# Optimization experiments

Hardware: AMD Instinct MI355X
Metric: run time of the kernel (lower is better)

Reference implementation:

```python
import jax, jax.numpy as jnp
import numpy as np

D, H, E, K, DF = 1024, 16, 8, 2, 4096
HD = D // H


def setup_inputs() -> dict:
    key = jax.random.key(0)
    ks = jax.random.split(key, 16)
    s = 0.02
    return {
        "x": jax.random.normal(ks[0], (8, 1024, D), jnp.float32),
        "ln1_g": jnp.ones((D,), jnp.float32),
        "ln1_b": jnp.zeros((D,), jnp.float32),
        "Wqkv": jax.random.normal(ks[1], (D, 3 * D), jnp.float32) * s,
        "bqkv": jnp.zeros((3 * D,), jnp.float32),
        "Wo": jax.random.normal(ks[2], (D, D), jnp.float32) * s,
        "bo": jnp.zeros((D,), jnp.float32),
        "ln2_g": jnp.ones((D,), jnp.float32),
        "ln2_b": jnp.zeros((D,), jnp.float32),
        "Wr": jax.random.normal(ks[3], (D, E), jnp.float32) * s,
        "W1": jax.random.normal(ks[4], (E, D, DF), jnp.float32) * s,
        "b1": jnp.zeros((E, DF), jnp.float32),
        "W2": jax.random.normal(ks[5], (E, DF, D), jnp.float32) * s,
        "b2": jnp.zeros((E, D), jnp.float32),
    }


def _ln(x, g, b, eps=1e-5):
    mu = jnp.mean(x, axis=-1, keepdims=True)
    var = jnp.var(x, axis=-1, keepdims=True)
    return (x - mu) * jax.lax.rsqrt(var + eps) * g + b


def reference(x, ln1_g, ln1_b, Wqkv, bqkv, Wo, bo, ln2_g, ln2_b, Wr, W1, b1, W2, b2):
    B, S, _ = x.shape
    # ---- pre-norm multi-head attention ----
    n1 = _ln(x, ln1_g, ln1_b)
    qkv = n1 @ Wqkv + bqkv  # [B,S,3D]
    q, k, v = jnp.split(qkv, 3, axis=-1)
    q = q.reshape(B, S, H, HD).transpose(0, 2, 1, 3)
    k = k.reshape(B, S, H, HD).transpose(0, 2, 1, 3)
    v = v.reshape(B, S, H, HD).transpose(0, 2, 1, 3)
    scores = jnp.einsum("bhqd,bhkd->bhqk", q, k) / np.sqrt(HD).astype(np.float32)
    attn = jax.nn.softmax(scores, axis=-1)
    ao = jnp.einsum("bhqk,bhkd->bhqd", attn, v)
    ao = ao.transpose(0, 2, 1, 3).reshape(B, S, D) @ Wo + bo
    x = x + ao  # residual (dropout=0)

    # ---- pre-norm MoE FFN ----
    n2 = _ln(x, ln2_g, ln2_b).reshape(B * S, D)  # [T,D]
    logits = n2 @ Wr  # [T,E]
    probs = jax.nn.softmax(logits, axis=-1)
    topv, topi = jax.lax.top_k(probs, K)  # [T,K]
    topv = topv / jnp.sum(topv, axis=-1, keepdims=True)
    onehot = jax.nn.one_hot(topi, E, dtype=probs.dtype)  # [T,K,E]
    gates = jnp.einsum("tke,tk->te", onehot, topv)  # dense sparse gates [T,E]

    # dense dispatch: each expert's FFN weighted by its gate (zero for unrouted)
    moe = jnp.zeros_like(n2)
    for e in range(E):
        h = jax.nn.gelu(n2 @ W1[e] + b1[e])
        moe = moe + gates[:, e:e + 1] * (h @ W2[e] + b2[e])
    x = x + moe.reshape(B, S, D)

    # load-balancing aux loss: E * sum(frac_routed_e * mean_prob_e)
    frac = jnp.mean(jnp.sum(onehot, axis=1), axis=0) / K  # [E]
    aux = E * jnp.sum(frac * jnp.mean(probs, axis=0))
    return x, aux
```

## Files before the change

kernel.cpp:

```cpp
#include <hip/hip_runtime.h>
#include <cstdint>
#include <cstddef>

using u16 = unsigned short;
using u32 = unsigned int;
typedef __attribute__((ext_vector_type(8))) short bf16x8;
typedef __attribute__((ext_vector_type(4))) float f32x4;

#define T_TOK 8192
#define SEQ   1024
#define NHEAD 16

__device__ __forceinline__ u16 f2b(float f) {
  u32 u = __float_as_uint(f);
  u32 r = (u + 0x7FFFu + ((u >> 16) & 1u)) >> 16;
  return (u16)r;
}
__device__ __forceinline__ float b2f(u16 u) {
  return __uint_as_float(((u32)u) << 16);
}
__device__ __forceinline__ u32 pk_bf16(float a, float b) {
  u32 r;
  asm("v_cvt_pk_bf16_f32 %0, %1, %2" : "=v"(r) : "v"(a), "v"(b));
  return r;
}

__global__ __launch_bounds__(256)
void k_cast_transpose(const float* __restrict__ in, u16* __restrict__ out, int R, int C) {
  __shared__ float tile[32][33];
  int bc = blockIdx.x * 32, br = blockIdx.y * 32;
  size_t bofs = (size_t)blockIdx.z * R * C;
  in += bofs; out += bofs;
  int tx = threadIdx.x, ty = threadIdx.y;
  for (int i = 0; i < 32; i += 8)
    tile[ty + i][tx] = in[(size_t)(br + ty + i) * C + bc + tx];
  __syncthreads();
  for (int i = 0; i < 32; i += 8)
    out[(size_t)(bc + ty + i) * R + br + tx] = f2b(tile[tx][ty + i]);
}

__global__ __launch_bounds__(256)
void k_ln(const float* __restrict__ x, const float* __restrict__ g, const float* __restrict__ b,
          u16* __restrict__ out) {
  int row = blockIdx.x, t = threadIdx.x;
  float4 v = ((const float4*)(x + (size_t)row * 1024))[t];
  float s  = v.x + v.y + v.z + v.w;
  float ss = v.x * v.x + v.y * v.y + v.z * v.z + v.w * v.w;
  for (int d = 1; d < 64; d <<= 1) { s += __shfl_xor(s, d); ss += __shfl_xor(ss, d); }
  __shared__ float sm[8];
  int w = t >> 6, lane = t & 63;
  if (lane == 0) { sm[w] = s; sm[4 + w] = ss; }
  __syncthreads();
  s = sm[0] + sm[1] + sm[2] + sm[3];
  ss = sm[4] + sm[5] + sm[6] + sm[7];
  float mu = s * (1.f / 1024.f);
  float var = ss * (1.f / 1024.f) - mu * mu;
  float inv = rsqrtf(var + 1e-5f);
  float4 gv = ((const float4*)g)[t];
  float4 bv = ((const float4*)b)[t];
  u32 lo = pk_bf16((v.x - mu) * inv * gv.x + bv.x, (v.y - mu) * inv * gv.y + bv.y);
  u32 hi = pk_bf16((v.z - mu) * inv * gv.z + bv.z, (v.w - mu) * inv * gv.w + bv.w);
  u32* dst = (u32*)(out + (size_t)row * 1024 + t * 4);
  dst[0] = lo; dst[1] = hi;
}

template<int MODE, bool EXPERT, bool GATHER>
__global__ __launch_bounds__(256)
void k_gemm(const u16* __restrict__ A, const u16* __restrict__ BT,
            const float* __restrict__ bias, const float* __restrict__ res,
            void* __restrict__ Cout, int M, int N, int Kd, int ldA,
            const int* __restrict__ off, const int* __restrict__ rows) {
  int nx = gridDim.x, ny = gridDim.y;
  int rid = blockIdx.x + nx * (blockIdx.y + ny * blockIdx.z);
  int z, bx, by;
  if (EXPERT) {
    z = rid & 7;
    int inner = rid >> 3;
    by = inner % ny;
    bx = inner / ny;
  } else {
    z = 0;
    int xcd = rid & 7;
    int inner = rid >> 3;
    bx = inner % nx;
    by = (inner / nx) * 8 + xcd;
  }
  int m_base = 0, M_local = M;
  if (EXPERT) { m_base = off[z]; M_local = off[z + 1] - m_base; }
  if (by * 128 >= M_local) return;
  if (EXPERT) { BT += (size_t)z * N * Kd; bias += (size_t)z * N; }

  __shared__ alignas(1024) u16 As[2][4096];
  __shared__ alignas(1024) u16 Bs[2][4096];

  int t = threadIdx.x;
  int lane = t & 63, w = t >> 6;
  int wm = w >> 1, wn = w & 1;
  int lr = lane & 15;
  int slot = lane >> 4;
  int sx = (slot ^ ((lr >> 1) & 3)) << 3;

  int ssrc = (lane & 3) ^ ((lane >> 3) & 3);
  const u16* aG[2]; const u16* bG[2];
  u16* aL[2]; u16* bL[2];
#pragma unroll
  for (int c = 0; c < 2; c++) {
    int chunk = 2 * w + c;
    int rl = chunk * 16 + (lane >> 2);
    int mr = by * 128 + rl;
    int mc = mr < M_local - 1 ? mr : M_local - 1;
    size_t arow = GATHER ? (size_t)rows[m_base + mc] : (size_t)(m_base + mc);
    aG[c] = A + arow * (size_t)ldA + ssrc * 8;
    bG[c] = BT + (size_t)(bx * 128 + rl) * Kd + ssrc * 8;
    aL[c] = &As[0][chunk * 512];
    bL[c] = &Bs[0][chunk * 512];
  }

  auto stage = [&](int k0, int buf) {
#pragma unroll
    for (int c = 0; c < 2; c++) {
      __builtin_amdgcn_global_load_lds(
          (const __attribute__((address_space(1))) void*)(aG[c] + k0),
          (__attribute__((address_space(3))) void*)(aL[c] + buf * 4096), 16, 0, 0);
      __builtin_amdgcn_global_load_lds(
          (const __attribute__((address_space(1))) void*)(bG[c] + k0),
          (__attribute__((address_space(3))) void*)(bL[c] + buf * 4096), 16, 0, 0);
    }
  };

  f32x4 acc[4][4] = {};

  stage(0, 0);
  __syncthreads();
  int cur = 0;
  for (int k0 = 0; k0 < Kd; k0 += 32) {
    if (k0 + 32 < Kd) stage(k0 + 32, cur ^ 1);
    bf16x8 af[4], bfr[4];
#pragma unroll
    for (int m = 0; m < 4; m++)
      af[m] = *(const bf16x8*)&As[cur][(wm * 64 + m * 16 + lr) * 32 + sx];
#pragma unroll
    for (int n = 0; n < 4; n++)
      bfr[n] = *(const bf16x8*)&Bs[cur][(wn * 64 + n * 16 + lr) * 32 + sx];
#pragma unroll
    for (int m = 0; m < 4; m++)
#pragma unroll
      for (int n = 0; n < 4; n++)
        acc[m][n] = __builtin_amdgcn_mfma_f32_16x16x32_bf16(af[m], bfr[n], acc[m][n], 0, 0, 0);
    __syncthreads();
    cur ^= 1;
  }

  int cr = (lane >> 4) * 4, cc = lane & 15;
#pragma unroll
  for (int m = 0; m < 4; m++) {
    int rl = by * 128 + wm * 64 + m * 16 + cr;
#pragma unroll
    for (int n = 0; n < 4; n++) {
      int col = bx * 128 + wn * 64 + n * 16 + cc;
      float bia = bias[col];
      float v0 = acc[m][n][0] + bia, v1 = acc[m][n][1] + bia;
      float v2 = acc[m][n][2] + bia, v3 = acc[m][n][3] + bia;
      if (MODE == 2) {
        const float cc2 = -2.3025850929940457f;
        float u0 = v0 + 0.044715f * v0 * v0 * v0;
        float u1 = v1 + 0.044715f * v1 * v1 * v1;
        float u2 = v2 + 0.044715f * v2 * v2 * v2;
        float u3 = v3 + 0.044715f * v3 * v3 * v3;
        v0 = v0 / (1.f + exp2f(cc2 * u0));
        v1 = v1 / (1.f + exp2f(cc2 * u1));
        v2 = v2 / (1.f + exp2f(cc2 * u2));
        v3 = v3 / (1.f + exp2f(cc2 * u3));
      }
      if (MODE == 0 || MODE == 2) {
        u32 p01 = pk_bf16(v0, v1), p23 = pk_bf16(v2, v3);
        u16* cp = (u16*)Cout;
        if (rl + 0 < M_local) cp[(size_t)(m_base + rl + 0) * N + col] = (u16)p01;
        if (rl + 1 < M_local) cp[(size_t)(m_base + rl + 1) * N + col] = (u16)(p01 >> 16);
        if (rl + 2 < M_local) cp[(size_t)(m_base + rl + 2) * N + col] = (u16)p23;
        if (rl + 3 < M_local) cp[(size_t)(m_base + rl + 3) * N + col] = (u16)(p23 >> 16);
      } else {
        float* cp = (float*)Cout;
        float vv[4] = {v0, v1, v2, v3};
#pragma unroll
        for (int r = 0; r < 4; r++) {
          int rr = rl + r;
          if (rr >= M_local) continue;
          size_t row = (size_t)(m_base + rr);
          if (MODE == 1) cp[row * N + col] = vv[r] + res[row * N + col];
          else           cp[row * N + col] = vv[r];
        }
      }
    }
  }
}

__global__ __launch_bounds__(256)
void k_attn(const u16* __restrict__ qkv, u16* __restrict__ ao) {
  __shared__ u16 Kt[64][72];
  __shared__ u16 Vt[64][72];
  __shared__ u16 Pl[4][16][72];

  int bh = blockIdx.y;
  int b = bh >> 4, h = bh & 15;
  int q0 = blockIdx.x * 64;
  int t = threadIdx.x, lane = t & 63, w = t >> 6;
  int lr = lane & 15, lk = (lane >> 4) * 8;

  int tq = b * SEQ + q0 + w * 16 + lr;
  const u16* qrow = qkv + (size_t)tq * 3072 + h * 64;
  bf16x8 qf[2];
#pragma unroll
  for (int kk = 0; kk < 2; kk++) {
    bf16x8 raw = *(const bf16x8*)(qrow + kk * 32 + lk);
#pragma unroll
    for (int j = 0; j < 8; j++) raw[j] = (short)f2b(b2f((u16)raw[j]) * 0.125f);
    qf[kk] = raw;
  }

  float m[4], l[4];
  f32x4 o[4];
#pragma unroll
  for (int r = 0; r < 4; r++) { m[r] = -1e30f; l[r] = 0.f; }
#pragma unroll
  for (int c = 0; c < 4; c++) o[c] = (f32x4){0.f, 0.f, 0.f, 0.f};

  int key_r = t >> 2;
  int key_c = (t & 3) * 16;

  for (int kv0 = 0; kv0 < SEQ; kv0 += 64) {
    int tk = b * SEQ + kv0 + key_r;
    const u16* krow = qkv + (size_t)tk * 3072 + 1024 + h * 64 + key_c;
    const u16* vrow = qkv + (size_t)tk * 3072 + 2048 + h * 64 + key_c;
    int4 ka = *(const int4*)krow;
    int4 kb = *(const int4*)(krow + 8);
    int4 vv4[2];
    vv4[0] = *(const int4*)vrow;
    vv4[1] = *(const int4*)(vrow + 8);
    const u16* vv = (const u16*)vv4;
    __syncthreads();
    *(int4*)&Kt[key_r][key_c] = ka;
    *(int4*)&Kt[key_r][key_c + 8] = kb;
#pragma unroll
    for (int j = 0; j < 16; j++) Vt[key_c + j][key_r] = vv[j];
    __syncthreads();

    f32x4 s[4];
#pragma unroll
    for (int n = 0; n < 4; n++) {
      s[n] = (f32x4){0.f, 0.f, 0.f, 0.f};
#pragma unroll
      for (int kk = 0; kk < 2; kk++) {
        bf16x8 kf = *(const bf16x8*)&Kt[n * 16 + lr][kk * 32 + lk];
        s[n] = __builtin_amdgcn_mfma_f32_16x16x32_bf16(qf[kk], kf, s[n], 0, 0, 0);
      }
    }
    float alpha[4], rsum[4];
#pragma unroll
    for (int r = 0; r < 4; r++) {
      float mx = fmaxf(fmaxf(s[0][r], s[1][r]), fmaxf(s[2][r], s[3][r]));
#pragma unroll
      for (int d = 1; d < 16; d <<= 1) mx = fmaxf(mx, __shfl_xor(mx, d));
      float mn = fmaxf(m[r], mx);
      alpha[r] = expf(m[r] - mn);
      m[r] = mn;
      rsum[r] = 0.f;
    }
#pragma unroll
    for (int n = 0; n < 4; n++)
#pragma unroll
      for (int r = 0; r < 4; r++) {
        float p = expf(s[n][r] - m[r]);
        rsum[r] += p;
        Pl[w][(lane >> 4) * 4 + r][n * 16 + lr] = f2b(p);
      }
#pragma unroll
    for (int r = 0; r < 4; r++) {
      float rs = rsum[r];
#pragma unroll
      for (int d = 1; d < 16; d <<= 1) rs += __shfl_xor(rs, d);
      l[r] = l[r] * alpha[r] + rs;
#pragma unroll
      for (int c = 0; c < 4; c++) o[c][r] *= alpha[r];
    }
    bf16x8 pa[2];
#pragma unroll
    for (int kk = 0; kk < 2; kk++) pa[kk] = *(const bf16x8*)&Pl[w][lr][kk * 32 + lk];
#pragma unroll
    for (int c = 0; c < 4; c++)
#pragma unroll
      for (int kk = 0; kk < 2; kk++) {
        bf16x8 vf = *(const bf16x8*)&Vt[c * 16 + lr][kk * 32 + lk];
        o[c] = __builtin_amdgcn_mfma_f32_16x16x32_bf16(pa[kk], vf, o[c], 0, 0, 0);
      }
  }

  int cr = (lane >> 4) * 4, cc = lane & 15;
#pragma unroll
  for (int r = 0; r < 4; r++) {
    float invl = 1.f / l[r];
    int trow = b * SEQ + q0 + w * 16 + cr + r;
#pragma unroll
    for (int c = 0; c < 4; c++)
      ao[(size_t)trow * 1024 + h * 64 + c * 16 + cc] = f2b(o[c][r] * invl);
  }
}

__global__ __launch_bounds__(256)
void k_router(const float* __restrict__ x1, const float* __restrict__ g, const float* __restrict__ b,
              const float* __restrict__ Wr, int* __restrict__ topi, float* __restrict__ topv,
              int* __restrict__ cnt_part, float* __restrict__ sp_part) {
  __shared__ int lcnt[8];
  __shared__ float lsp[8];
  int t = threadIdx.x, w = t >> 6, lane = t & 63;
  if (t < 8) { lcnt[t] = 0; lsp[t] = 0.f; }
  __syncthreads();

  float gv[16], bv[16];
#pragma unroll
  for (int i = 0; i < 4; i++) {
    float4 g4 = ((const float4*)g)[lane * 4 + i];
    float4 b4 = ((const float4*)b)[lane * 4 + i];
    gv[i * 4 + 0] = g4.x; gv[i * 4 + 1] = g4.y; gv[i * 4 + 2] = g4.z; gv[i * 4 + 3] = g4.w;
    bv[i * 4 + 0] = b4.x; bv[i * 4 + 1] = b4.y; bv[i * 4 + 2] = b4.z; bv[i * 4 + 3] = b4.w;
  }
  float wr[16][8];
#pragma unroll
  for (int j = 0; j < 16; j++) {
    float4 w0 = ((const float4*)Wr)[(lane * 16 + j) * 2];
    float4 w1 = ((const float4*)Wr)[(lane * 16 + j) * 2 + 1];
    wr[j][0] = w0.x; wr[j][1] = w0.y; wr[j][2] = w0.z; wr[j][3] = w0.w;
    wr[j][4] = w1.x; wr[j][5] = w1.y; wr[j][6] = w1.z; wr[j][7] = w1.w;
  }

  for (int i = 0; i < 8; i++) {
    int row = blockIdx.x * 32 + w * 8 + i;
    const float4* xr = (const float4*)(x1 + (size_t)row * 1024);
    float xv[16];
    float s = 0.f, ss = 0.f;
#pragma unroll
    for (int q = 0; q < 4; q++) {
      float4 v = xr[lane * 4 + q];
      xv[q * 4 + 0] = v.x; xv[q * 4 + 1] = v.y; xv[q * 4 + 2] = v.z; xv[q * 4 + 3] = v.w;
      s += v.x + v.y + v.z + v.w;
      ss += v.x * v.x + v.y * v.y + v.z * v.z + v.w * v.w;
    }
#pragma unroll
    for (int d = 1; d < 64; d <<= 1) { s += __shfl_xor(s, d); ss += __shfl_xor(ss, d); }
    float mu = s * (1.f / 1024.f);
    float var = ss * (1.f / 1024.f) - mu * mu;
    float inv = rsqrtf(var + 1e-5f);
    float p[8] = {};
#pragma unroll
    for (int j = 0; j < 16; j++) {
      float n = (xv[j] - mu) * inv * gv[j] + bv[j];
#pragma unroll
      for (int e = 0; e < 8; e++) p[e] += n * wr[j][e];
    }
#pragma unroll
    for (int e = 0; e < 8; e++)
#pragma unroll
      for (int d = 1; d < 64; d <<= 1) p[e] += __shfl_xor(p[e], d);
    if (lane == 0) {
      float mx = p[0];
#pragma unroll
      for (int e = 1; e < 8; e++) mx = fmaxf(mx, p[e]);
      float ex[8], sum = 0.f;
#pragma unroll
      for (int e = 0; e < 8; e++) { ex[e] = expf(p[e] - mx); sum += ex[e]; }
      float pr[8];
#pragma unroll
      for (int e = 0; e < 8; e++) pr[e] = ex[e] / sum;
      int i0 = 0; float b0 = pr[0];
      for (int e = 1; e < 8; e++) if (pr[e] > b0) { b0 = pr[e]; i0 = e; }
      int i1 = -1; float b1 = -1.f;
      for (int e = 0; e < 8; e++) if (e != i0 && pr[e] > b1) { b1 = pr[e]; i1 = e; }
      float inv2 = 1.f / (b0 + b1);
      topi[row * 2] = i0; topi[row * 2 + 1] = i1;
      topv[row * 2] = b0 * inv2; topv[row * 2 + 1] = b1 * inv2;
      atomicAdd(&lcnt[i0], 1); atomicAdd(&lcnt[i1], 1);
#pragma unroll
      for (int e = 0; e < 8; e++) atomicAdd(&lsp[e], pr[e]);
    }
  }
  __syncthreads();
  if (t < 8) {
    cnt_part[blockIdx.x * 8 + t] = lcnt[t];
    sp_part[blockIdx.x * 8 + t] = lsp[t];
  }
}

__global__ void k_scan_aux(const int* __restrict__ cnt_part, const float* __restrict__ sp_part,
                           int* __restrict__ off, int* __restrict__ cursor, float* __restrict__ aux_out) {
  __shared__ int csum[8];
  __shared__ float ssum[8];
  int t = threadIdx.x;
  int e = t & 7, ch = t >> 3;
  int c = 0; float s = 0.f;
  for (int i = ch * 32; i < ch * 32 + 32; i++) { c += cnt_part[i * 8 + e]; s += sp_part[i * 8 + e]; }
#pragma unroll
  for (int d = 8; d < 64; d <<= 1) { c += __shfl_xor(c, d); s += __shfl_xor(s, d); }
  if (t < 8) { csum[t] = c; ssum[t] = s; }
  __syncthreads();
  if (t == 0) {
    int o = 0;
    for (int q = 0; q < 8; q++) { off[q] = o; cursor[q] = o; o += csum[q]; }
    off[8] = o;
    float aux = 0.f;
    for (int q = 0; q < 8; q++)
      aux += ((float)csum[q] / (float)(T_TOK * 2)) * (ssum[q] / (float)T_TOK);
    aux_out[0] = 8.f * aux;
  }
}

__global__ __launch_bounds__(256)
void k_scatter(const int* __restrict__ topi, int* __restrict__ cursor,
               int* __restrict__ rows, int* __restrict__ slot_of) {
  __shared__ int hist[8];
  __shared__ int base[8];
  int t = threadIdx.x;
  if (t < 8) hist[t] = 0;
  __syncthreads();
  int tok = blockIdx.x * 256 + t;
  int e0 = topi[tok * 2], e1 = topi[tok * 2 + 1];
  int r0 = atomicAdd(&hist[e0], 1);
  int r1 = atomicAdd(&hist[e1], 1);
  __syncthreads();
  if (t < 8) base[t] = atomicAdd(&cursor[t], hist[t]);
  __syncthreads();
  int p0 = base[e0] + r0, p1 = base[e1] + r1;
  rows[p0] = tok; rows[p1] = tok;
  slot_of[tok * 2] = p0; slot_of[tok * 2 + 1] = p1;
}

__global__ __launch_bounds__(256)
void k_combine(const float* __restrict__ x1, const float* __restrict__ out2,
               const int* __restrict__ slot_of, const float* __restrict__ topv,
               float* __restrict__ out) {
  int row = blockIdx.x, t = threadIdx.x;
  int s0 = slot_of[row * 2], s1 = slot_of[row * 2 + 1];
  float w0 = topv[row * 2], w1 = topv[row * 2 + 1];
  float4 a  = ((const float4*)(x1 + (size_t)row * 1024))[t];
  float4 e0 = ((const float4*)(out2 + (size_t)s0 * 1024))[t];
  float4 e1 = ((const float4*)(out2 + (size_t)s1 * 1024))[t];
  float4 r;
  r.x = a.x + w0 * e0.x + w1 * e1.x;
  r.y = a.y + w0 * e0.y + w1 * e1.y;
  r.z = a.z + w0 * e0.z + w1 * e1.z;
  r.w = a.w + w0 * e0.w + w1 * e1.w;
  ((float4*)(out + (size_t)row * 1024))[t] = r;
}

extern "C" void kernel_launch(void* const* d_in, const int* in_sizes, int n_in,
                              void* d_out, int out_size, void* d_ws, size_t ws_size,
                              hipStream_t stream) {
  const float* x    = (const float*)d_in[0];
  const float* ln1g = (const float*)d_in[1];
  const float* ln1b = (const float*)d_in[2];
  const float* Wqkv = (const float*)d_in[3];
  const float* bqkv = (const float*)d_in[4];
  const float* Wo   = (const float*)d_in[5];
  const float* bo   = (const float*)d_in[6];
  const float* ln2g = (const float*)d_in[7];
  const float* ln2b = (const float*)d_in[8];
  const float* Wr   = (const float*)d_in[9];
  const float* W1   = (const float*)d_in[10];
  const float* b1   = (const float*)d_in[11];
  const float* W2   = (const float*)d_in[12];
  const float* b2   = (const float*)d_in[13];
  float* out = (float*)d_out;

  char* wp = (char*)d_ws;
  auto alloc = [&](size_t bytes) -> void* {
    void* p = (void*)wp;
    wp += (bytes + 255) & ~(size_t)255;
    return p;
  };
  u16*   WqkvT = (u16*)alloc((size_t)3072 * 1024 * 2);
  u16*   WoT   = (u16*)alloc((size_t)1024 * 1024 * 2);
  u16*   W1T   = (u16*)alloc((size_t)8 * 4096 * 1024 * 2);
  u16*   W2T   = (u16*)alloc((size_t)8 * 1024 * 4096 * 2);
  u16*   n1    = (u16*)alloc((size_t)8192 * 1024 * 2);
  u16*   qkv   = (u16*)alloc((size_t)8192 * 3072 * 2);
  u16*   aob   = (u16*)alloc((size_t)8192 * 1024 * 2);
  float* x1    = (float*)alloc((size_t)8192 * 1024 * 4);
  u16*   n2b   = (u16*)alloc((size_t)8192 * 1024 * 2);
  u16*   hbuf  = (u16*)alloc((size_t)16384 * 4096 * 2);
  float* out2  = (float*)alloc((size_t)16384 * 1024 * 4);
  int*   topi  = (int*)alloc((size_t)8192 * 2 * 4);
  float* topv  = (float*)alloc((size_t)8192 * 2 * 4);
  int*   rowsl = (int*)alloc((size_t)16384 * 4);
  int*   slot  = (int*)alloc((size_t)16384 * 4);
  int*   cntp  = (int*)alloc((size_t)256 * 8 * 4);
  float* spp   = (float*)alloc((size_t)256 * 8 * 4);
  int*   offs  = (int*)alloc(256);
  int*   curs  = (int*)alloc(256);

  k_cast_transpose<<<dim3(96, 32, 1), dim3(32, 8), 0, stream>>>(Wqkv, WqkvT, 1024, 3072);
  k_cast_transpose<<<dim3(32, 32, 1), dim3(32, 8), 0, stream>>>(Wo, WoT, 1024, 1024);
  k_cast_transpose<<<dim3(128, 32, 8), dim3(32, 8), 0, stream>>>(W1, W1T, 1024, 4096);
  k_cast_transpose<<<dim3(32, 128, 8), dim3(32, 8), 0, stream>>>(W2, W2T, 4096, 1024);

  k_ln<<<8192, 256, 0, stream>>>(x, ln1g, ln1b, n1);
  k_gemm<0, false, false><<<dim3(24, 64, 1), 256, 0, stream>>>(
      n1, WqkvT, bqkv, nullptr, qkv, 8192, 3072, 1024, 1024, nullptr, nullptr);
  k_attn<<<dim3(16, 128), 256, 0, stream>>>(qkv, aob);
  k_gemm<1, false, false><<<dim3(8, 64, 1), 256, 0, stream>>>(
      aob, WoT, bo, x, x1, 8192, 1024, 1024, 1024, nullptr, nullptr);

  k_ln<<<8192, 256, 0, stream>>>(x1, ln2g, ln2b, n2b);
  k_router<<<256, 256, 0, stream>>>(x1, ln2g, ln2b, Wr, topi, topv, cntp, spp);
  k_scan_aux<<<1, 64, 0, stream>>>(cntp, spp, offs, curs, out + 8388608);
  k_scatter<<<32, 256, 0, stream>>>(topi, curs, rowsl, slot);

  k_gemm<2, true, true><<<dim3(32, 64, 8), 256, 0, stream>>>(
      n2b, W1T, b1, nullptr, hbuf, 0, 4096, 1024, 1024, offs, rowsl);
  k_gemm<3, true, false><<<dim3(8, 64, 8), 256, 0, stream>>>(
      hbuf, W2T, b2, nullptr, out2, 0, 1024, 4096, 4096, offs, nullptr);
  k_combine<<<8192, 256, 0, stream>>>(x1, out2, slot, topv, out);
}
```

Before: 905.5 us.

## Fuse LN2 into router and make expert GEMMs loop over row tiles

The second LayerNorm is folded into the router kernel, which now writes the normalized bf16 activations while computing routing logits, removing a separate pass over x1. The GEMM kernel gains an outer loop over M-tiles with a grid stride, so the expert GEMMs launch a quarter as many row blocks and each block walks several row tiles. This cuts the many early-exit blocks for lightly loaded experts, at the cost of less parallelism and load imbalance when one expert gets many tokens.

```diff
diff --git a/kernel.cpp b/kernel.cpp
--- a/kernel.cpp
+++ b/kernel.cpp
@@ -72,22 +72,23 @@
             const int* __restrict__ off, const int* __restrict__ rows) {
   int nx = gridDim.x, ny = gridDim.y;
   int rid = blockIdx.x + nx * (blockIdx.y + ny * blockIdx.z);
-  int z, bx, by;
+  int z, bx, by0, bystep;
   if (EXPERT) {
     z = rid & 7;
     int inner = rid >> 3;
-    by = inner % ny;
+    by0 = inner % ny;
     bx = inner / ny;
+    bystep = ny;
   } else {
     z = 0;
     int xcd = rid & 7;
     int inner = rid >> 3;
     bx = inner % nx;
-    by = (inner / nx) * 8 + xcd;
+    by0 = (inner / nx) * 8 + xcd;
+    bystep = 1 << 20;
   }
   int m_base = 0, M_local = M;
   if (EXPERT) { m_base = off[z]; M_local = off[z + 1] - m_base; }
-  if (by * 128 >= M_local) return;
   if (EXPERT) { BT += (size_t)z * N * Kd; bias += (size_t)z * N; }
 
   __shared__ alignas(1024) u16 As[2][4096];
@@ -101,94 +102,100 @@
   int sx = (slot ^ ((lr >> 1) & 3)) << 3;
 
   int ssrc = (lane & 3) ^ ((lane >> 3) & 3);
-  const u16* aG[2]; const u16* bG[2];
-  u16* aL[2]; u16* bL[2];
+  const u16* bG[2];
+  int rlc[2], cofs[2];
 #pragma unroll
   for (int c = 0; c < 2; c++) {
     int chunk = 2 * w + c;
-    int rl = chunk * 16 + (lane >> 2);
-    int mr = by * 128 + rl;
-    int mc = mr < M_local - 1 ? mr : M_local - 1;
-    size_t arow = GATHER ? (size_t)rows[m_base + mc] : (size_t)(m_base + mc);
-    aG[c] = A + arow * (size_t)ldA + ssrc * 8;
-    bG[c] = BT + (size_t)(bx * 128 + rl) * Kd + ssrc * 8;
-    aL[c] = &As[0][chunk * 512];
-    bL[c] = &Bs[0][chunk * 512];
-  }
-
-  auto stage = [&](int k0, int buf) {
+    rlc[c] = chunk * 16 + (lane >> 2);
+    bG[c] = BT + (size_t)(bx * 128 + rlc[c]) * Kd + ssrc * 8;
+    cofs[c] = chunk * 512;
+  }
+
+  for (int by = by0; by * 128 < M_local; by += bystep) {
+    const u16* aG[2];
 #pragma unroll
     for (int c = 0; c < 2; c++) {
-      __builtin_amdgcn_global_load_lds(
-          (const __attribute__((address_space(1))) void*)(aG[c] + k0),
-          (__attribute__((address_space(3))) void*)(aL[c] + buf * 4096), 16, 0, 0);
-      __builtin_amdgcn_global_load_lds(
-          (const __attribute__((address_space(1))) void*)(bG[c] + k0),
-          (__attribute__((address_space(3))) void*)(bL[c] + buf * 4096), 16, 0, 0);
-    }
-  };
-
-  f32x4 acc[4][4] = {};
-
-  stage(0, 0);
-  __syncthreads();
-  int cur = 0;
-  for (int k0 = 0; k0 < Kd; k0 += 32) {
-    if (k0 + 32 < Kd) stage(k0 + 32, cur ^ 1);
-    bf16x8 af[4], bfr[4];
-#pragma unroll
-    for (int m = 0; m < 4; m++)
-      af[m] = *(const bf16x8*)&As[cur][(wm * 64 + m * 16 + lr) * 32 + sx];
-#pragma unroll
-    for (int n = 0; n < 4; n++)
-      bfr[n] = *(const bf16x8*)&Bs[cur][(wn * 64 + n * 16 + lr) * 32 + sx];
-#pragma unroll
-    for (int m = 0; m < 4; m++)
+      int mr = by * 128 + rlc[c];
+      int mc = mr < M_local - 1 ? mr : M_local - 1;
+      size_t arow = GATHER ? (size_t)rows[m_base + mc] : (size_t)(m_base + mc);
+      aG[c] = A + arow * (size_t)ldA + ssrc * 8;
+    }
+
+    auto stage = [&](int k0, int buf) {
+#pragma unroll
+      for (int c = 0; c < 2; c++) {
+        __builtin_amdgcn_global_load_lds(
+            (const __attribute__((address_space(1))) void*)(aG[c] + k0),
+            (__attribute__((address_space(3))) void*)(&As[buf][cofs[c]]), 16, 0, 0);
+        __builtin_amdgcn_global_load_lds(
+            (const __attribute__((address_space(1))) void*)(bG[c] + k0),
+            (__attribute__((address_space(3))) void*)(&Bs[buf][cofs[c]]), 16, 0, 0);
+      }
+    };
+
+    f32x4 acc[4][4] = {};
+
+    stage(0, 0);
+    __syncthreads();
+    int cur = 0;
+    for (int k0 = 0; k0 < Kd; k0 += 32) {
+      if (k0 + 32 < Kd) stage(k0 + 32, cur ^ 1);
+      bf16x8 af[4], bfr[4];
+#pragma unroll
+      for (int m = 0; m < 4; m++)
+        af[m] = *(const bf16x8*)&As[cur][(wm * 64 + m * 16 + lr) * 32 + sx];
 #pragma unroll
       for (int n = 0; n < 4; n++)
-        acc[m][n] = __builtin_amdgcn_mfma_f32_16x16x32_bf16(af[m], bfr[n], acc[m][n], 0, 0, 0);
-    __syncthreads();
-    cur ^= 1;
-  }
-
-  int cr = (lane >> 4) * 4, cc = lane & 15;
-#pragma unroll
-  for (int m = 0; m < 4; m++) {
-    int rl = by * 128 + wm * 64 + m * 16 + cr;
-#pragma unroll
-    for (int n = 0; n < 4; n++) {
-      int col = bx * 128 + wn * 64 + n * 16 + cc;
-      float bia = bias[col];
-      float v0 = acc[m][n][0] + bia, v1 = acc[m][n][1] + bia;
-      float v2 = acc[m][n][2] + bia, v3 = acc[m][n][3] + bia;
-      if (MODE == 2) {
-        const float cc2 = -2.3025850929940457f;
-        float u0 = v0 + 0.044715f * v0 * v0 * v0;
-        float u1 = v1 + 0.044715f * v1 * v1 * v1;
-        float u2 = v2 + 0.044715f * v2 * v2 * v2;
-        float u3 = v3 + 0.044715f * v3 * v3 * v3;
-        v0 = v0 / (1.f + exp2f(cc2 * u0));
-        v1 = v1 / (1.f + exp2f(cc2 * u1));
-        v2 = v2 / (1.f + exp2f(cc2 * u2));
-        v3 = v3 / (1.f + exp2f(cc2 * u3));
-      }
-      if (MODE == 0 || MODE == 2) {
-        u32 p01 = pk_bf16(v0, v1), p23 = pk_bf16(v2, v3);
-        u16* cp = (u16*)Cout;
-        if (rl + 0 < M_local) cp[(size_t)(m_base + rl + 0) * N + col] = (u16)p01;
-        if (rl + 1 < M_local) cp[(size_t)(m_base + rl + 1) * N + col] = (u16)(p01 >> 16);
-        if (rl + 2 < M_local) cp[(size_t)(m_base + rl + 2) * N + col] = (u16)p23;
-        if (rl + 3 < M_local) cp[(size_t)(m_base + rl + 3) * N + col] = (u16)(p23 >> 16);
-      } else {
-        float* cp = (float*)Cout;
-        float vv[4] = {v0, v1, v2, v3};
-#pragma unroll
-        for (int r = 0; r < 4; r++) {
-          int rr = rl + r;
-          if (rr >= M_local) continue;
-          size_t row = (size_t)(m_base + rr);
-          if (MODE == 1) cp[row * N + col] = vv[r] + res[row * N + col];
-          else           cp[row * N + col] = vv[r];
+        bfr[n] = *(const bf16x8*)&Bs[cur][(wn * 64 + n * 16 + lr) * 32 + sx];
+#pragma unroll
+      for (int m = 0; m < 4; m++)
+#pragma unroll
+        for (int n = 0; n < 4; n++)
+          acc[m][n] = __builtin_amdgcn_mfma_f32_16x16x32_bf16(af[m], bfr[n], acc[m][n], 0, 0, 0);
+      __syncthreads();
+      cur ^= 1;
+    }
+
+    int cr = (lane >> 4) * 4, cc = lane & 15;
+#pragma unroll
+    for (int m = 0; m < 4; m++) {
+      int rl = by * 128 + wm * 64 + m * 16 + cr;
+#pragma unroll
+      for (int n = 0; n < 4; n++) {
+        int col = bx * 128 + wn * 64 + n * 16 + cc;
+        float bia = bias[col];
+        float v0 = acc[m][n][0] + bia, v1 = acc[m][n][1] + bia;
+        float v2 = acc[m][n][2] + bia, v3 = acc[m][n][3] + bia;
+        if (MODE == 2) {
+          const float cc2 = -2.3025850929940457f;
+          float u0 = v0 + 0.044715f * v0 * v0 * v0;
+          float u1 = v1 + 0.044715f * v1 * v1 * v1;
+          float u2 = v2 + 0.044715f * v2 * v2 * v2;
+          float u3 = v3 + 0.044715f * v3 * v3 * v3;
+          v0 = v0 / (1.f + exp2f(cc2 * u0));
+          v1 = v1 / (1.f + exp2f(cc2 * u1));
+          v2 = v2 / (1.f + exp2f(cc2 * u2));
+          v3 = v3 / (1.f + exp2f(cc2 * u3));
+        }
+        if (MODE == 0 || MODE == 2) {
+          u32 p01 = pk_bf16(v0, v1), p23 = pk_bf16(v2, v3);
+          u16* cp = (u16*)Cout;
+          if (rl + 0 < M_local) cp[(size_t)(m_base + rl + 0) * N + col] = (u16)p01;
+          if (rl + 1 < M_local) cp[(size_t)(m_base + rl + 1) * N + col] = (u16)(p01 >> 16);
+          if (rl + 2 < M_local) cp[(size_t)(m_base + rl + 2) * N + col] = (u16)p23;
+          if (rl + 3 < M_local) cp[(size_t)(m_base + rl + 3) * N + col] = (u16)(p23 >> 16);
+        } else {
+          float* cp = (float*)Cout;
+          float vv[4] = {v0, v1, v2, v3};
+#pragma unroll
+          for (int r = 0; r < 4; r++) {
+            int rr = rl + r;
+            if (rr >= M_local) continue;
+            size_t row = (size_t)(m_base + rr);
+            if (MODE == 1) cp[row * N + col] = vv[r] + res[row * N + col];
+            else           cp[row * N + col] = vv[r];
+          }
         }
       }
     }
@@ -308,7 +315,8 @@
 
 __global__ __launch_bounds__(256)
 void k_router(const float* __restrict__ x1, const float* __restrict__ g, const float* __restrict__ b,
-              const float* __restrict__ Wr, int* __restrict__ topi, float* __restrict__ topv,
+              const float* __restrict__ Wr, u16* __restrict__ n2b,
+              int* __restrict__ topi, float* __restrict__ topv,
               int* __restrict__ cnt_part, float* __restrict__ sp_part) {
   __shared__ int lcnt[8];
   __shared__ float lsp[8];
@@ -354,8 +362,17 @@
 #pragma unroll
     for (int j = 0; j < 16; j++) {
       float n = (xv[j] - mu) * inv * gv[j] + bv[j];
+      xv[j] = n;
 #pragma unroll
       for (int e = 0; e < 8; e++) p[e] += n * wr[j][e];
+    }
+    {
+      u32 pk[8];
+#pragma unroll
+      for (int jj = 0; jj < 8; jj++) pk[jj] = pk_bf16(xv[2 * jj], xv[2 * jj + 1]);
+      uint4* dst = (uint4*)(n2b + (size_t)row * 1024 + lane * 16);
+      dst[0] = make_uint4(pk[0], pk[1], pk[2], pk[3]);
+      dst[1] = make_uint4(pk[4], pk[5], pk[6], pk[7]);
     }
 #pragma unroll
     for (int e = 0; e < 8; e++)
@@ -508,14 +525,13 @@
   k_gemm<1, false, false><<<dim3(8, 64, 1), 256, 0, stream>>>(
       aob, WoT, bo, x, x1, 8192, 1024, 1024, 1024, nullptr, nullptr);
 
-  k_ln<<<8192, 256, 0, stream>>>(x1, ln2g, ln2b, n2b);
-  k_router<<<256, 256, 0, stream>>>(x1, ln2g, ln2b, Wr, topi, topv, cntp, spp);
+  k_router<<<256, 256, 0, stream>>>(x1, ln2g, ln2b, Wr, n2b, topi, topv, cntp, spp);
   k_scan_aux<<<1, 64, 0, stream>>>(cntp, spp, offs, curs, out + 8388608);
   k_scatter<<<32, 256, 0, stream>>>(topi, curs, rowsl, slot);
 
-  k_gemm<2, true, true><<<dim3(32, 64, 8), 256, 0, stream>>>(
+  k_gemm<2, true, true><<<dim3(32, 16, 8), 256, 0, stream>>>(
       n2b, W1T, b1, nullptr, hbuf, 0, 4096, 1024, 1024, offs, rowsl);
-  k_gemm<3, true, false><<<dim3(8, 64, 8), 256, 0, stream>>>(
+  k_gemm<3, true, false><<<dim3(8, 16, 8), 256, 0, stream>>>(
       hbuf, W2T, b2, nullptr, out2, 0, 1024, 4096, 4096, offs, nullptr);
   k_combine<<<8192, 256, 0, stream>>>(x1, out2, slot, topv, out);
 }
```

New measurement: 1.042 ms. +15.1%, slower.

## Fuse LN2 bf16 output into router and store expert outputs as bf16

Applied to the files above, without the earlier changes.

The router kernel now writes the normalized bf16 activations itself, so the separate second layernorm launch and its extra read of x1 go away. The second expert GEMM switches to epilogue mode 0 and writes bf16 instead of fp32, halving the out2 buffer. The combine kernel reads the bf16 expert outputs and widens them. This cuts memory traffic in exchange for lower precision in the expert outputs, and mode 0 may add a bias differently than mode 3 did.

```diff
diff --git a/kernel.cpp b/kernel.cpp
--- a/kernel.cpp
+++ b/kernel.cpp
@@ -308,7 +308,8 @@
 
 __global__ __launch_bounds__(256)
 void k_router(const float* __restrict__ x1, const float* __restrict__ g, const float* __restrict__ b,
-              const float* __restrict__ Wr, int* __restrict__ topi, float* __restrict__ topv,
+              const float* __restrict__ Wr, u16* __restrict__ n2b,
+              int* __restrict__ topi, float* __restrict__ topv,
               int* __restrict__ cnt_part, float* __restrict__ sp_part) {
   __shared__ int lcnt[8];
   __shared__ float lsp[8];
@@ -354,8 +355,17 @@
 #pragma unroll
     for (int j = 0; j < 16; j++) {
       float n = (xv[j] - mu) * inv * gv[j] + bv[j];
+      xv[j] = n;
 #pragma unroll
       for (int e = 0; e < 8; e++) p[e] += n * wr[j][e];
+    }
+    {
+      u32 pk[8];
+#pragma unroll
+      for (int jj = 0; jj < 8; jj++) pk[jj] = pk_bf16(xv[2 * jj], xv[2 * jj + 1]);
+      uint4* dst = (uint4*)(n2b + (size_t)row * 1024 + lane * 16);
+      dst[0] = make_uint4(pk[0], pk[1], pk[2], pk[3]);
+      dst[1] = make_uint4(pk[4], pk[5], pk[6], pk[7]);
     }
 #pragma unroll
     for (int e = 0; e < 8; e++)
@@ -434,20 +444,20 @@
 }
 
 __global__ __launch_bounds__(256)
-void k_combine(const float* __restrict__ x1, const float* __restrict__ out2,
+void k_combine(const float* __restrict__ x1, const u16* __restrict__ out2,
                const int* __restrict__ slot_of, const float* __restrict__ topv,
                float* __restrict__ out) {
   int row = blockIdx.x, t = threadIdx.x;
   int s0 = slot_of[row * 2], s1 = slot_of[row * 2 + 1];
   float w0 = topv[row * 2], w1 = topv[row * 2 + 1];
-  float4 a  = ((const float4*)(x1 + (size_t)row * 1024))[t];
-  float4 e0 = ((const float4*)(out2 + (size_t)s0 * 1024))[t];
-  float4 e1 = ((const float4*)(out2 + (size_t)s1 * 1024))[t];
+  float4 a = ((const float4*)(x1 + (size_t)row * 1024))[t];
+  ushort4 e0 = ((const ushort4*)(out2 + (size_t)s0 * 1024))[t];
+  ushort4 e1 = ((const ushort4*)(out2 + (size_t)s1 * 1024))[t];
   float4 r;
-  r.x = a.x + w0 * e0.x + w1 * e1.x;
-  r.y = a.y + w0 * e0.y + w1 * e1.y;
-  r.z = a.z + w0 * e0.z + w1 * e1.z;
-  r.w = a.w + w0 * e0.w + w1 * e1.w;
+  r.x = a.x + w0 * b2f(e0.x) + w1 * b2f(e1.x);
+  r.y = a.y + w0 * b2f(e0.y) + w1 * b2f(e1.y);
+  r.z = a.z + w0 * b2f(e0.z) + w1 * b2f(e1.z);
+  r.w = a.w + w0 * b2f(e0.w) + w1 * b2f(e1.w);
   ((float4*)(out + (size_t)row * 1024))[t] = r;
 }
 
@@ -486,7 +496,7 @@
   float* x1    = (float*)alloc((size_t)8192 * 1024 * 4);
   u16*   n2b   = (u16*)alloc((size_t)8192 * 1024 * 2);
   u16*   hbuf  = (u16*)alloc((size_t)16384 * 4096 * 2);
-  float* out2  = (float*)alloc((size_t)16384 * 1024 * 4);
+  u16*   out2  = (u16*)alloc((size_t)16384 * 1024 * 2);
   int*   topi  = (int*)alloc((size_t)8192 * 2 * 4);
   float* topv  = (float*)alloc((size_t)8192 * 2 * 4);
   int*   rowsl = (int*)alloc((size_t)16384 * 4);
@@ -508,14 +518,13 @@
   k_gemm<1, false, false><<<dim3(8, 64, 1), 256, 0, stream>>>(
       aob, WoT, bo, x, x1, 8192, 1024, 1024, 1024, nullptr, nullptr);
 
-  k_ln<<<8192, 256, 0, stream>>>(x1, ln2g, ln2b, n2b);
-  k_router<<<256, 256, 0, stream>>>(x1, ln2g, ln2b, Wr, topi, topv, cntp, spp);
+  k_router<<<256, 256, 0, stream>>>(x1, ln2g, ln2b, Wr, n2b, topi, topv, cntp, spp);
   k_scan_aux<<<1, 64, 0, stream>>>(cntp, spp, offs, curs, out + 8388608);
   k_scatter<<<32, 256, 0, stream>>>(topi, curs, rowsl, slot);
 
   k_gemm<2, true, true><<<dim3(32, 64, 8), 256, 0, stream>>>(
       n2b, W1T, b1, nullptr, hbuf, 0, 4096, 1024, 1024, offs, rowsl);
-  k_gemm<3, true, false><<<dim3(8, 64, 8), 256, 0, stream>>>(
+  k_gemm<0, true, false><<<dim3(8, 64, 8), 256, 0, stream>>>(
       hbuf, W2T, b2, nullptr, out2, 0, 1024, 4096, 4096, offs, nullptr);
   k_combine<<<8192, 256, 0, stream>>>(x1, out2, slot, topv, out);
 }
```

Result: faster. 882.0 us (-2.6%).
